# Optimization experiments

Hardware: AMD Instinct MI355X
Metric: run time of the kernel (lower is better)

## Reference

```python
import jax, jax.numpy as jnp
import numpy as np

BN, T, D_MODEL = 128, 256, 128
D_INNER, D_STATE, D_CONV, DT_RANK = 2 * D_MODEL, 16, 4, 8  # mamba-ssm defaults


def silu(v):
    return v * jax.nn.sigmoid(v)


def setup_inputs() -> dict:
    key = jax.random.key(0)
    ks = jax.random.split(key, 8)
    s = 0.02
    A_log = jnp.log(jnp.tile(jnp.arange(1, D_STATE + 1, dtype=jnp.float32), (D_INNER, 1)))
    return {
        "x": jax.random.normal(ks[0], (BN, T, D_MODEL), jnp.float32),
        "in_proj_w": jax.random.normal(ks[1], (2 * D_INNER, D_MODEL), jnp.float32) * s,
        "conv_w": jax.random.normal(ks[2], (D_INNER, 1, D_CONV), jnp.float32) * s,
        "conv_b": jnp.zeros((D_INNER,), jnp.float32),
        "x_proj_w": jax.random.normal(ks[3], (DT_RANK + 2 * D_STATE, D_INNER), jnp.float32) * s,
        "dt_proj_w": jax.random.normal(ks[4], (D_INNER, DT_RANK), jnp.float32) * s,
        "dt_proj_b": jax.random.uniform(ks[5], (D_INNER,), jnp.float32, -4.0, -2.0),
        "A_log": A_log,
        "D": jnp.ones((D_INNER,), jnp.float32),
        "out_proj_w": jax.random.normal(ks[6], (D_MODEL, D_INNER), jnp.float32) * s,
        "down_w": jax.random.normal(ks[7], (D_MODEL, D_MODEL, 3), jnp.float32) * s,
        "down_b": jnp.zeros((D_MODEL,), jnp.float32),
        "ln_g": jnp.ones((D_MODEL,), jnp.float32),
        "ln_b": jnp.zeros((D_MODEL,), jnp.float32),
    }


def _mamba(x, in_proj_w, conv_w, conv_b, x_proj_w, dt_proj_w, dt_proj_b, A_log, D, out_proj_w):
    B = x.shape[0]
    xz = jnp.einsum('bld,ed->ble', x, in_proj_w)            # (B,L,2*di)
    xc, z = jnp.split(xz, 2, axis=-1)
    # depthwise causal conv over time
    xt = xc.transpose(0, 2, 1)                               # (B,di,L)
    xt = jax.lax.conv_general_dilated(xt, conv_w, (1,), [(D_CONV - 1, 0)],
                                      feature_group_count=D_INNER)
    xc = silu((xt + conv_b[None, :, None]).transpose(0, 2, 1))  # (B,L,di)
    x_dbl = jnp.einsum('bld,ed->ble', xc, x_proj_w)
    dt, Bm, Cm = jnp.split(x_dbl, [DT_RANK, DT_RANK + D_STATE], axis=-1)
    delta = jax.nn.softplus(jnp.einsum('blr,dr->bld', dt, dt_proj_w) + dt_proj_b)  # (B,L,di)
    A = -jnp.exp(A_log)                                       # (di,N)

    def step(h, inp):
        d_t, B_t, C_t, u_t = inp                              # (B,di),(B,N),(B,N),(B,di)
        dA = jnp.exp(d_t[..., None] * A)                      # (B,di,N)
        h = dA * h + (d_t * u_t)[..., None] * B_t[:, None, :]
        return h, jnp.einsum('bdn,bn->bd', h, C_t)

    h0 = jnp.zeros((B, D_INNER, D_STATE), x.dtype)
    _, ys = jax.lax.scan(step, h0, (delta.swapaxes(0, 1), Bm.swapaxes(0, 1),
                                    Cm.swapaxes(0, 1), xc.swapaxes(0, 1)))
    y = ys.swapaxes(0, 1) + xc * D                            # (B,L,di)
    y = y * silu(z)
    return jnp.einsum('ble,de->bld', y, out_proj_w)


def reference(x, in_proj_w, conv_w, conv_b, x_proj_w, dt_proj_w, dt_proj_b,
              A_log, D, out_proj_w, down_w, down_b, ln_g, ln_b):
    x_skip = x
    h = _mamba(x, in_proj_w, conv_w, conv_b, x_proj_w, dt_proj_w, dt_proj_b,
               A_log, D, out_proj_w)                          # dropout: eval mode = identity
    ht = h.transpose(0, 2, 1)                                 # (B,d,T)
    ht = jax.lax.conv_general_dilated(ht, down_w, (2,), [(1, 1)]) + down_b[None, :, None]
    h = ht.transpose(0, 2, 1)                                 # (B,T//2,d)
    mu = jnp.mean(h, axis=-1, keepdims=True)
    var = jnp.mean((h - mu) ** 2, axis=-1, keepdims=True)
    h = (h - mu) * jax.lax.rsqrt(var + 1e-5) * ln_g + ln_b
    return (h, x_skip)
```

## Files before the change

### kernel.cpp

```cpp
#include <hip/hip_runtime.h>
#include <hip/hip_bf16.h>


typedef __attribute__((ext_vector_type(8))) short bf16x8;
typedef __attribute__((ext_vector_type(4))) short bf16x4;
typedef __attribute__((ext_vector_type(4))) float f32x4;
using bf16 = __hip_bfloat16;

static __device__ __forceinline__ short f2s(float v) {
  union { bf16 b; short s; } u; u.b = (bf16)v; return u.s;
}
static __device__ __forceinline__ float s2f(short s) {
  union { short s; bf16 b; } u; u.s = s; return (float)u.b;
}

__global__ __launch_bounds__(256) void prep_all(const float* __restrict__ x,
                                                const float* __restrict__ ipw,
                                                const float* __restrict__ xpw,
                                                const float* __restrict__ dwn,
                                                const float* __restrict__ opw,
                                                short* __restrict__ xb,
                                                float* __restrict__ out1,
                                                short* __restrict__ ipwb,
                                                short* __restrict__ wxb,
                                                short* __restrict__ G) {
  const int bid = blockIdx.x;
  if (bid < 4096) {
    int i = (bid * 256 + threadIdx.x) * 4;
    f32x4 v = *(const f32x4*)(x + i);
    bf16x4 o;
    o[0] = f2s(v[0]); o[1] = f2s(v[1]); o[2] = f2s(v[2]); o[3] = f2s(v[3]);
    *(bf16x4*)(xb + i) = o;
    *(f32x4*)(out1 + i) = v;
  } else if (bid < 4416) {
    int idx = (bid - 4096) * 256 + threadIdx.x;
    if (idx < 65536) {
      ipwb[idx] = f2s(ipw[idx]);
    } else {
      int j = idx - 65536;
      int n = j >> 8;
      wxb[j] = (n < 40) ? f2s(xpw[j]) : (short)0;
    }
  } else {
    const int jb = bid - 4416;
    const int k  = jb >> 7;
    const int co = jb & 127;
    const int e  = threadIdx.x;
    float acc = 0.f;
    for (int dm = 0; dm < 128; ++dm) {
      acc += dwn[(co * 128 + dm) * 3 + k] * opw[dm * 256 + e];
    }
    G[(size_t)(k * 128 + co) * 256 + e] = f2s(acc);
  }
}

__global__ __launch_bounds__(256) void inproj_k(const short* __restrict__ A,
                                                const short* __restrict__ W,
                                                short* __restrict__ xcpreT,
                                                short* __restrict__ zTb) {
  const int m_base = blockIdx.x * 64;
  const int n_base = blockIdx.y * 64;
  const int wave = threadIdx.x >> 6;
  const int lane = threadIdx.x & 63;
  const int r16  = lane & 15;
  const int quad = lane >> 4;
  f32x4 acc[4] = {};
  const short* Ap = A + (size_t)(m_base + wave * 16 + r16) * 128 + quad * 8;
  const short* Wp = W + (size_t)(n_base + r16) * 128 + quad * 8;
#pragma unroll
  for (int k0 = 0; k0 < 128; k0 += 32) {
    bf16x8 a = *(const bf16x8*)(Ap + k0);
#pragma unroll
    for (int j = 0; j < 4; ++j) {
      bf16x8 b = *(const bf16x8*)(Wp + (size_t)j * 16 * 128 + k0);
      acc[j] = __builtin_amdgcn_mfma_f32_16x16x32_bf16(a, b, acc[j], 0, 0, 0);
    }
  }
  __shared__ short LT[64][72];
  const bool isz = (n_base >= 256);
#pragma unroll
  for (int j = 0; j < 4; ++j) {
#pragma unroll
    for (int r = 0; r < 4; ++r) {
      float v = acc[j][r];
      short s = isz ? f2s(v / (1.f + __expf(-v))) : f2s(v);
      LT[j * 16 + r16][wave * 16 + quad * 4 + r] = s;
    }
  }
  __syncthreads();
  const int bb = m_base >> 8;
  const int tbase = m_base & 255;
  short* dst = isz ? zTb : xcpreT;
  const int dbase = isz ? (n_base - 256) : n_base;
#pragma unroll
  for (int it = 0; it < 2; ++it) {
    const int dw = (threadIdx.x >> 3) + it * 32;
    const int tc = (threadIdx.x & 7) * 8;
    bf16x8 v = *(const bf16x8*)(&LT[dw][tc]);
    *(bf16x8*)(dst + (size_t)(bb * 256 + dbase + dw) * 256 + tbase + tc) = v;
  }
}

__global__ __launch_bounds__(256, 4) void mid_k(const short* __restrict__ xcpreT,
                                                const float* __restrict__ cw,
                                                const float* __restrict__ cb,
                                                const short* __restrict__ wxb,
                                                const float* __restrict__ dtw,
                                                const float* __restrict__ dtb,
                                                short* __restrict__ xcT,
                                                short* __restrict__ dT,
                                                float* __restrict__ SBC) {
  const int b  = blockIdx.x >> 3;
  const int t0 = (blockIdx.x & 7) * 32;
  const int tg = threadIdx.x >> 6;
  const int dl = threadIdx.x & 63;
  const int tA = t0 + tg * 8;
  __shared__ short XC[32][264];
  __shared__ float DTL[32][8];
#pragma unroll
  for (int dtile = 0; dtile < 4; ++dtile) {
    const int d = dtile * 64 + dl;
    const float w0 = cw[d * 4], w1 = cw[d * 4 + 1];
    const float w2 = cw[d * 4 + 2], w3 = cw[d * 4 + 3];
    const float bias = cb[d];
    const size_t base = ((size_t)b * 256 + d) * 256;
    bf16x8 v = *(const bf16x8*)(xcpreT + base + tA);
    bf16x8 hp = {};
    if (tA >= 8) hp = *(const bf16x8*)(xcpreT + base + tA - 8);
    float x3 = s2f(hp[5]), x2 = s2f(hp[6]), x1 = s2f(hp[7]);
    bf16x8 outv;
#pragma unroll
    for (int i = 0; i < 8; ++i) {
      const float cur = s2f(v[i]);
      const float a = bias + x3 * w0 + x2 * w1 + x1 * w2 + cur * w3;
      const short s = f2s(a / (1.f + __expf(-a)));
      outv[i] = s;
      XC[tg * 8 + i][d] = s;
      x3 = x2; x2 = x1; x1 = cur;
    }
    *(bf16x8*)(xcT + base + tA) = outv;
  }
  __syncthreads();
  if (tg < 3) {
    const int r16  = dl & 15;
    const int quad = dl >> 4;
    f32x4 acc0 = {}, acc1 = {};
    const short* Wp = wxb + (size_t)(tg * 16 + r16) * 256 + quad * 8;
#pragma unroll
    for (int k0 = 0; k0 < 256; k0 += 32) {
      bf16x8 bb = *(const bf16x8*)(Wp + k0);
      bf16x8 a0 = *(const bf16x8*)(&XC[r16][quad * 8 + k0]);
      bf16x8 a1 = *(const bf16x8*)(&XC[16 + r16][quad * 8 + k0]);
      acc0 = __builtin_amdgcn_mfma_f32_16x16x32_bf16(a0, bb, acc0, 0, 0, 0);
      acc1 = __builtin_amdgcn_mfma_f32_16x16x32_bf16(a1, bb, acc1, 0, 0, 0);
    }
    const int col = tg * 16 + r16;
#pragma unroll
    for (int r = 0; r < 4; ++r) {
      const int tl0 = quad * 4 + r;
      const int tl1 = 16 + quad * 4 + r;
      if (col < 8) {
        DTL[tl0][col] = acc0[r];
        DTL[tl1][col] = acc1[r];
      } else if (col < 40) {
        SBC[((size_t)b * 256 + t0 + tl0) * 32 + (col - 8)] = acc0[r];
        SBC[((size_t)b * 256 + t0 + tl1) * 32 + (col - 8)] = acc1[r];
      }
    }
  }
  __syncthreads();
#pragma unroll
  for (int dtile = 0; dtile < 4; ++dtile) {
    const int d = dtile * 64 + dl;
    float wd[8];
#pragma unroll
    for (int j = 0; j < 8; ++j) wd[j] = dtw[d * 8 + j];
    const float bd = dtb[d];
    const size_t base = ((size_t)b * 256 + d) * 256;
    bf16x8 dv;
#pragma unroll
    for (int i = 0; i < 8; ++i) {
      const int tl = tg * 8 + i;
      const f32x4 p0 = *(const f32x4*)(&DTL[tl][0]);
      const f32x4 p1 = *(const f32x4*)(&DTL[tl][4]);
      float acc = bd;
#pragma unroll
      for (int j = 0; j < 4; ++j) acc += p0[j] * wd[j] + p1[j] * wd[4 + j];
      const float delta = (acc > 20.f) ? acc : __logf(1.f + __expf(acc));
      dv[i] = f2s(delta);
    }
    *(bf16x8*)(dT + base + tA) = dv;
  }
}

#define LDS_S(SB, CH) do {                                                   \
    _Pragma("unroll")                                                        \
    for (int j_ = 0; j_ < 8; ++j_) {                                         \
      SBr[SB][j_] = *(const f32x4*)(&S[(CH) * 8 + j_][q * 4]);               \
      SCr[SB][j_] = *(const f32x4*)(&S[(CH) * 8 + j_][16 + q * 4]);          \
    }                                                                        \
  } while (0)

#define LDG(GB, CH) do {                                                     \
    if ((CH) < 32) {                                                         \
      uu[GB] = *(const bf16x8*)(xcT + tb + (size_t)(CH) * 8);                \
      dd[GB] = *(const bf16x8*)(dT + tb + (size_t)(CH) * 8);                 \
      if (q == 0) zz[GB] = *(const bf16x8*)(zT + tb + (size_t)(CH) * 8);     \
    }                                                                        \
  } while (0)

#define CHUNK(GB, SB, CH) do {                                               \
    _Pragma("unroll")                                                        \
    for (int tt_ = 0; tt_ < 8; ++tt_) {                                      \
      const int t_ = (CH) * 8 + tt_;                                         \
      const float delta_ = s2f(dd[GB][tt_]);                                 \
      const float u_ = s2f(uu[GB][tt_]);                                     \
      const float du_ = delta_ * u_;                                         \
      const f32x4 Bq_ = SBr[SB][tt_];                                        \
      const f32x4 Cq_ = SCr[SB][tt_];                                        \
      float yt_ = 0.f;                                                       \
      _Pragma("unroll")                                                      \
      for (int n_ = 0; n_ < 4; ++n_) {                                       \
        const float dA_ = __builtin_amdgcn_exp2f(delta_ * A2[n_]);           \
        h[n_] = dA_ * h[n_] + du_ * Bq_[n_];                                 \
        yt_ += h[n_] * Cq_[n_];                                              \
      }                                                                      \
      yt_ += __shfl_xor(yt_, 1);                                             \
      yt_ += __shfl_xor(yt_, 2);                                             \
      if (q == 0)                                                            \
        yb[(rb + t_) * 256 + d] = f2s((yt_ + u_ * Dv) * s2f(zz[GB][tt_]));   \
    }                                                                        \
  } while (0)

__global__ __launch_bounds__(128, 2) void scan10(const float* __restrict__ SBC,
                                                 const short* __restrict__ xcT,
                                                 const short* __restrict__ dT,
                                                 const short* __restrict__ zT,
                                                 const float* __restrict__ alog,
                                                 const float* __restrict__ Dp,
                                                 short* __restrict__ yb) {
  const int g = blockIdx.x & 7;
  const int b = blockIdx.x >> 3;
  const int q = threadIdx.x & 3;
  const int d = g * 32 + (threadIdx.x >> 2);
  const size_t rb = (size_t)b * 256;
  __shared__ float S[256][32];
  for (int i = threadIdx.x; i < 2048; i += 128) {
    *(f32x4*)(&S[i >> 3][(i & 7) * 4]) =
        *(const f32x4*)(SBC + (size_t)b * 8192 + i * 4);
  }
  float A2[4];
#pragma unroll
  for (int n = 0; n < 4; ++n)
    A2[n] = -__expf(alog[d * 16 + q * 4 + n]) * 1.44269504089f;
  const float Dv = Dp[d];
  float h[4] = {0.f, 0.f, 0.f, 0.f};
  const size_t tb = ((size_t)b * 256 + d) * 256;
  f32x4 SBr[2][8], SCr[2][8];
  bf16x8 uu[4], dd[4];
  bf16x8 zz[4] = {};
  LDG(0, 0); LDG(1, 1); LDG(2, 2); LDG(3, 3);
  __syncthreads();
  LDS_S(0, 0);
  for (int c = 0; c < 32; c += 4) {
    LDS_S(1, c + 1);
    CHUNK(0, 0, c);
    LDG(0, c + 4);
    LDS_S(0, c + 2);
    CHUNK(1, 1, c + 1);
    LDG(1, c + 5);
    LDS_S(1, c + 3);
    CHUNK(2, 0, c + 2);
    LDG(2, c + 6);
    if (c + 4 < 32) LDS_S(0, c + 4);
    CHUNK(3, 1, c + 3);
    LDG(3, c + 7);
  }
}

__global__ __launch_bounds__(256) void od_k(const short* __restrict__ yb,
                                            const short* __restrict__ G,
                                            const float* __restrict__ db,
                                            const float* __restrict__ lng,
                                            const float* __restrict__ lnb,
                                            float* __restrict__ out) {
  const int wave = threadIdx.x >> 6;
  const int lane = threadIdx.x & 63;
  const int r16  = lane & 15;
  const int quad = lane >> 4;
  const int m_base = blockIdx.x * 64 + wave * 16;
  const int ma = m_base + r16;
  const int ba = ma >> 7, toa = ma & 127;
  f32x4 acc[8] = {};
  const bf16x8 az = {};
#pragma unroll
  for (int k = 0; k < 3; ++k) {
    const int tp = 2 * toa + k - 1;
    const bool valid = (tp >= 0) && (tp < 256);
    const int tpc = tp < 0 ? 0 : (tp > 255 ? 255 : tp);
    const short* Ap = yb + (size_t)(ba * 256 + tpc) * 256 + quad * 8;
    const short* Gp = G + (size_t)(k * 128 + r16) * 256 + quad * 8;
#pragma unroll
    for (int k0 = 0; k0 < 256; k0 += 32) {
      bf16x8 a = *(const bf16x8*)(Ap + k0);
      a = valid ? a : az;
#pragma unroll
      for (int j = 0; j < 8; ++j) {
        bf16x8 g = *(const bf16x8*)(Gp + (size_t)j * 16 * 256 + k0);
        acc[j] = __builtin_amdgcn_mfma_f32_16x16x32_bf16(a, g, acc[j], 0, 0, 0);
      }
    }
  }
  float dbv[8], g8[8], be8[8];
#pragma unroll
  for (int j = 0; j < 8; ++j) {
    const int col = j * 16 + r16;
    dbv[j] = db[col]; g8[j] = lng[col]; be8[j] = lnb[col];
  }
#pragma unroll
  for (int r = 0; r < 4; ++r) {
    float v[8];
    float s = 0.f;
#pragma unroll
    for (int j = 0; j < 8; ++j) { v[j] = acc[j][r] + dbv[j]; s += v[j]; }
    s += __shfl_xor(s, 1); s += __shfl_xor(s, 2);
    s += __shfl_xor(s, 4); s += __shfl_xor(s, 8);
    const float mu = s * (1.0f / 128.0f);
    float vs = 0.f;
#pragma unroll
    for (int j = 0; j < 8; ++j) { const float dd = v[j] - mu; vs += dd * dd; }
    vs += __shfl_xor(vs, 1); vs += __shfl_xor(vs, 2);
    vs += __shfl_xor(vs, 4); vs += __shfl_xor(vs, 8);
    const float rstd = rsqrtf(vs * (1.0f / 128.0f) + 1e-5f);
    const int rowm = m_base + quad * 4 + r;
#pragma unroll
    for (int j = 0; j < 8; ++j) {
      out[(size_t)rowm * 128 + j * 16 + r16] = (v[j] - mu) * rstd * g8[j] + be8[j];
    }
  }
}

static const size_t O_XCPRE = 0;
static const size_t O_XCT   = 16777216;
static const size_t O_ZT    = 33554432;
static const size_t O_DT    = 50331648;
static const size_t O_SBC   = 67108864;
static const size_t O_G     = 71303168;
static const size_t O_XB    = 75497472;
static const size_t O_IPWB  = 92274688;

extern "C" void kernel_launch(void* const* d_in, const int* in_sizes, int n_in,
                              void* d_out, int out_size, void* d_ws, size_t ws_size,
                              hipStream_t stream) {
  const float* x    = (const float*)d_in[0];
  const float* ipw  = (const float*)d_in[1];
  const float* cw   = (const float*)d_in[2];
  const float* cb   = (const float*)d_in[3];
  const float* xpw  = (const float*)d_in[4];
  const float* dtw  = (const float*)d_in[5];
  const float* dtb  = (const float*)d_in[6];
  const float* alog = (const float*)d_in[7];
  const float* Dp   = (const float*)d_in[8];
  const float* opw  = (const float*)d_in[9];
  const float* dw   = (const float*)d_in[10];
  const float* db   = (const float*)d_in[11];
  const float* lng  = (const float*)d_in[12];
  const float* lnb  = (const float*)d_in[13];

  char*  ws     = (char*)d_ws;
  short* xcpreT = (short*)(ws + O_XCPRE);
  short* yb     = (short*)(ws + O_XCPRE);
  short* xcT    = (short*)(ws + O_XCT);
  short* zT     = (short*)(ws + O_ZT);
  short* dT     = (short*)(ws + O_DT);
  float* SBC    = (float*)(ws + O_SBC);
  short* G      = (short*)(ws + O_G);
  short* xb     = (short*)(ws + O_XB);
  short* ipwb   = (short*)(ws + O_IPWB);
  float* out    = (float*)d_out;
  short* wxb    = (short*)out;
  float* out1   = out + 2097152;

  prep_all<<<4800, 256, 0, stream>>>(x, ipw, xpw, dw, opw,
                                     xb, out1, ipwb, wxb, G);
  inproj_k<<<dim3(512, 8), 256, 0, stream>>>(xb, ipwb, xcpreT, zT);
  mid_k<<<1024, 256, 0, stream>>>(xcpreT, cw, cb, wxb, dtw, dtb,
                                  xcT, dT, SBC);
  scan10<<<1024, 128, 0, stream>>>(SBC, xcT, dT, zT, alog, Dp, yb);
  od_k<<<256, 256, 0, stream>>>(yb, G, db, lng, lnb, out);
}
```

Baseline: 247.0 us.

## Tile xc, delta, z into scan-friendly packed layout and stage y through LDS

```diff
diff --git a/kernel.cpp b/kernel.cpp
--- a/kernel.cpp
+++ b/kernel.cpp
@@ -12,6 +12,10 @@
 }
 static __device__ __forceinline__ float s2f(short s) {
   union { short s; bf16 b; } u; u.s = s; return (float)u.b;
+}
+
+static __device__ __forceinline__ size_t pidx(int b, int d, int t) {
+  return ((((size_t)b * 8 + (d >> 5)) * 32 + (t >> 3)) * 32 + (d & 31)) * 8 + (t & 7);
 }
 
 __global__ __launch_bounds__(256) void prep_all(const float* __restrict__ x,
@@ -57,7 +61,7 @@
 __global__ __launch_bounds__(256) void inproj_k(const short* __restrict__ A,
                                                 const short* __restrict__ W,
                                                 short* __restrict__ xcpreT,
-                                                short* __restrict__ zTb) {
+                                                short* __restrict__ zP) {
   const int m_base = blockIdx.x * 64;
   const int n_base = blockIdx.y * 64;
   const int wave = threadIdx.x >> 6;
@@ -90,14 +94,19 @@
   __syncthreads();
   const int bb = m_base >> 8;
   const int tbase = m_base & 255;
-  short* dst = isz ? zTb : xcpreT;
   const int dbase = isz ? (n_base - 256) : n_base;
 #pragma unroll
   for (int it = 0; it < 2; ++it) {
     const int dw = (threadIdx.x >> 3) + it * 32;
     const int tc = (threadIdx.x & 7) * 8;
     bf16x8 v = *(const bf16x8*)(&LT[dw][tc]);
-    *(bf16x8*)(dst + (size_t)(bb * 256 + dbase + dw) * 256 + tbase + tc) = v;
+    const int d = dbase + dw;
+    const int t = tbase + tc;
+    if (isz) {
+      *(bf16x8*)(zP + pidx(bb, d, t)) = v;
+    } else {
+      *(bf16x8*)(xcpreT + ((size_t)(bb * 256 + d)) * 256 + t) = v;
+    }
   }
 }
 
@@ -107,8 +116,8 @@
                                                 const short* __restrict__ wxb,
                                                 const float* __restrict__ dtw,
                                                 const float* __restrict__ dtb,
-                                                short* __restrict__ xcT,
-                                                short* __restrict__ dT,
+                                                short* __restrict__ xcP,
+                                                short* __restrict__ dP,
                                                 float* __restrict__ SBC) {
   const int b  = blockIdx.x >> 3;
   const int t0 = (blockIdx.x & 7) * 32;
@@ -138,7 +147,7 @@
       XC[tg * 8 + i][d] = s;
       x3 = x2; x2 = x1; x1 = cur;
     }
-    *(bf16x8*)(xcT + base + tA) = outv;
+    *(bf16x8*)(xcP + pidx(b, d, tA)) = outv;
   }
   __syncthreads();
   if (tg < 3) {
@@ -176,7 +185,6 @@
 #pragma unroll
     for (int j = 0; j < 8; ++j) wd[j] = dtw[d * 8 + j];
     const float bd = dtb[d];
-    const size_t base = ((size_t)b * 256 + d) * 256;
     bf16x8 dv;
 #pragma unroll
     for (int i = 0; i < 8; ++i) {
@@ -189,7 +197,7 @@
       const float delta = (acc > 20.f) ? acc : __logf(1.f + __expf(acc));
       dv[i] = f2s(delta);
     }
-    *(bf16x8*)(dT + base + tA) = dv;
+    *(bf16x8*)(dP + pidx(b, d, tA)) = dv;
   }
 }
 
@@ -203,9 +211,9 @@
 
 #define LDG(GB, CH) do {                                                     \
     if ((CH) < 32) {                                                         \
-      uu[GB] = *(const bf16x8*)(xcT + tb + (size_t)(CH) * 8);                \
-      dd[GB] = *(const bf16x8*)(dT + tb + (size_t)(CH) * 8);                 \
-      if (q == 0) zz[GB] = *(const bf16x8*)(zT + tb + (size_t)(CH) * 8);     \
+      uu[GB] = *(const bf16x8*)(xcP + pb + (size_t)(CH) * 256);              \
+      dd[GB] = *(const bf16x8*)(dP + pb + (size_t)(CH) * 256);               \
+      if (q == 0) zz[GB] = *(const bf16x8*)(zP + pb + (size_t)(CH) * 256);   \
     }                                                                        \
   } while (0)
 
@@ -228,23 +236,25 @@
       yt_ += __shfl_xor(yt_, 1);                                             \
       yt_ += __shfl_xor(yt_, 2);                                             \
       if (q == 0)                                                            \
-        yb[(rb + t_) * 256 + d] = f2s((yt_ + u_ * Dv) * s2f(zz[GB][tt_]));   \
+        Y[t_][dl] = f2s((yt_ + u_ * Dv) * s2f(zz[GB][tt_]));                 \
     }                                                                        \
   } while (0)
 
-__global__ __launch_bounds__(128, 2) void scan10(const float* __restrict__ SBC,
-                                                 const short* __restrict__ xcT,
-                                                 const short* __restrict__ dT,
-                                                 const short* __restrict__ zT,
+__global__ __launch_bounds__(128, 2) void scan11(const float* __restrict__ SBC,
+                                                 const short* __restrict__ xcP,
+                                                 const short* __restrict__ dP,
+                                                 const short* __restrict__ zP,
                                                  const float* __restrict__ alog,
                                                  const float* __restrict__ Dp,
                                                  short* __restrict__ yb) {
   const int g = blockIdx.x & 7;
   const int b = blockIdx.x >> 3;
   const int q = threadIdx.x & 3;
-  const int d = g * 32 + (threadIdx.x >> 2);
+  const int dl = threadIdx.x >> 2;
+  const int d = g * 32 + dl;
   const size_t rb = (size_t)b * 256;
   __shared__ float S[256][32];
+  __shared__ short Y[256][32];
   for (int i = threadIdx.x; i < 2048; i += 128) {
     *(f32x4*)(&S[i >> 3][(i & 7) * 4]) =
         *(const f32x4*)(SBC + (size_t)b * 8192 + i * 4);
@@ -255,7 +265,7 @@
     A2[n] = -__expf(alog[d * 16 + q * 4 + n]) * 1.44269504089f;
   const float Dv = Dp[d];
   float h[4] = {0.f, 0.f, 0.f, 0.f};
-  const size_t tb = ((size_t)b * 256 + d) * 256;
+  const size_t pb = (((size_t)b * 8 + g) * 32) * 256 + (size_t)dl * 8;
   f32x4 SBr[2][8], SCr[2][8];
   bf16x8 uu[4], dd[4];
   bf16x8 zz[4] = {};
@@ -276,6 +286,15 @@
     CHUNK(3, 1, c + 3);
     LDG(3, c + 7);
   }
+  __syncthreads();
+#pragma unroll
+  for (int r = 0; r < 8; ++r) {
+    const int f = (r * 128 + threadIdx.x) * 8;
+    const int t = f >> 5;
+    const int d0 = f & 31;
+    bf16x8 v = *(const bf16x8*)(&Y[t][d0]);
+    *(bf16x8*)(yb + (rb + t) * 256 + g * 32 + d0) = v;
+  }
 }
 
 __global__ __launch_bounds__(256) void od_k(const short* __restrict__ yb,
@@ -341,9 +360,9 @@
 }
 
 static const size_t O_XCPRE = 0;
-static const size_t O_XCT   = 16777216;
-static const size_t O_ZT    = 33554432;
-static const size_t O_DT    = 50331648;
+static const size_t O_XCP   = 16777216;
+static const size_t O_ZP    = 33554432;
+static const size_t O_DP    = 50331648;
 static const size_t O_SBC   = 67108864;
 static const size_t O_G     = 71303168;
 static const size_t O_XB    = 75497472;
@@ -370,9 +389,9 @@
   char*  ws     = (char*)d_ws;
   short* xcpreT = (short*)(ws + O_XCPRE);
   short* yb     = (short*)(ws + O_XCPRE);
-  short* xcT    = (short*)(ws + O_XCT);
-  short* zT     = (short*)(ws + O_ZT);
-  short* dT     = (short*)(ws + O_DT);
+  short* xcP    = (short*)(ws + O_XCP);
+  short* zP     = (short*)(ws + O_ZP);
+  short* dP     = (short*)(ws + O_DP);
   float* SBC    = (float*)(ws + O_SBC);
   short* G      = (short*)(ws + O_G);
   short* xb     = (short*)(ws + O_XB);
@@ -383,9 +402,9 @@
 
   prep_all<<<4800, 256, 0, stream>>>(x, ipw, xpw, dw, opw,
                                      xb, out1, ipwb, wxb, G);
-  inproj_k<<<dim3(512, 8), 256, 0, stream>>>(xb, ipwb, xcpreT, zT);
+  inproj_k<<<dim3(512, 8), 256, 0, stream>>>(xb, ipwb, xcpreT, zP);
   mid_k<<<1024, 256, 0, stream>>>(xcpreT, cw, cb, wxb, dtw, dtb,
-                                  xcT, dT, SBC);
-  scan10<<<1024, 128, 0, stream>>>(SBC, xcT, dT, zT, alog, Dp, yb);
+                                  xcP, dP, SBC);
+  scan11<<<1024, 128, 0, stream>>>(SBC, xcP, dP, zP, alog, Dp, yb);
   od_k<<<256, 256, 0, stream>>>(yb, G, db, lng, lnb, out);
 }
```

New measurement: 293.5 us. +18.8%, slower.
